# Kernel optimization log

Measured on AMD Instinct MI355X. Metric: run time of the kernel, lower is better.

## Reference

```python
import jax, jax.numpy as jnp
import numpy as np

DIM = 1024        # BIGNET_DIM
GS = 16           # group_size
N_LAYERS = 18     # 6 blocks * 3 QLoRALinear
N_BLOCKS = 6
R = 32            # lora_dim
B = 32768         # flattened batch/tokens
LN_EPS = 1e-5


def _qlora_linear(x, qw, sc, b, la, lb):
    # Dequantize int4 weights: per-group (group_size=16 along in_features) scale.
    O, I = qw.shape
    w = (qw.astype(jnp.float32).reshape(O, I // GS, GS) * sc[:, :, None]).reshape(O, I)
    base = x @ w.T + b                      # [B, O] dequant-matmul
    lora = (x @ la.T) @ lb.T                # fp32 low-rank branch [B,R]->[B,O]
    return base + lora


def _layernorm(x, g, b):
    mu = jnp.mean(x, axis=-1, keepdims=True)
    var = jnp.mean((x - mu) ** 2, axis=-1, keepdims=True)
    return (x - mu) * jax.lax.rsqrt(var + LN_EPS) * g + b


def setup_inputs() -> dict:
    key = jax.random.key(0)
    ks = jax.random.split(key, 6)
    x = jax.random.normal(ks[0], (B, DIM), dtype=jnp.float32)
    # int4 codes in [-8, 7]
    qw = jax.random.randint(ks[1], (N_LAYERS, DIM, DIM), -8, 8, dtype=jnp.int32)
    # positive per-group scales (absmax/7-like magnitude)
    scales = jax.random.uniform(ks[2], (N_LAYERS, DIM, DIM // GS), dtype=jnp.float32,
                                minval=0.005, maxval=0.02)
    bias = 0.02 * jax.random.normal(ks[3], (N_LAYERS, DIM), dtype=jnp.float32)
    lora_a = (1.0 / np.sqrt(DIM)) * jax.random.normal(ks[4], (N_LAYERS, R, DIM), dtype=jnp.float32)
    # lora_b is zero-init in the module; use small random values so the branch is exercised
    lora_b = 0.01 * jax.random.normal(ks[5], (N_LAYERS, DIM, R), dtype=jnp.float32)
    ln_g = jnp.ones((N_BLOCKS - 1, DIM), dtype=jnp.float32)
    ln_b = jnp.zeros((N_BLOCKS - 1, DIM), dtype=jnp.float32)
    return {"x": x, "qw": qw, "scales": scales, "bias": bias,
            "lora_a": lora_a, "lora_b": lora_b, "ln_g": ln_g, "ln_b": ln_b}


def reference(x, qw, scales, bias, lora_a, lora_b, ln_g, ln_b):
    h = x
    for blk in range(N_BLOCKS):
        y = h
        for j in range(3):
            li = blk * 3 + j
            y = _qlora_linear(y, qw[li], scales[li], bias[li], lora_a[li], lora_b[li])
            if j < 2:
                y = jax.nn.relu(y)
        h = y + h                     # residual
        if blk < N_BLOCKS - 1:
            h = _layernorm(h, ln_g[blk], ln_b[blk])
    return h
```

## Files before the change

### kernel.cpp

```cpp
#include <hip/hip_runtime.h>
#include <cstdint>

typedef _Float16 f16;
typedef _Float16 f16x8 __attribute__((ext_vector_type(8)));
typedef _Float16 f16x4 __attribute__((ext_vector_type(4)));
typedef float    f32x4 __attribute__((ext_vector_type(4)));

#define DIMN 1024
#define BATCH 32768
#define NLAYERS 18
#define NBLOCKS 6

__device__ __forceinline__ void gl2lds16(const f16* g, const f16* l) {
    auto gp = (const __attribute__((address_space(1))) unsigned int*)(uintptr_t)g;
    auto lp = (__attribute__((address_space(3))) unsigned int*)(uintptr_t)l;
    __builtin_amdgcn_global_load_lds(gp, lp, 16, 0, 0);
}

__global__ void cvt_kernel(const float* __restrict__ x, f16* __restrict__ o) {
    int i = (blockIdx.x * 256 + threadIdx.x) * 4;
    float4 v = *(const float4*)&x[i];
    f16x4 r;
    r[0] = (f16)v.x; r[1] = (f16)v.y; r[2] = (f16)v.z; r[3] = (f16)v.w;
    *(f16x4*)&o[i] = r;
}

__global__ __launch_bounds__(256) void prep_w_kernel(
        const int* __restrict__ qw, const float* __restrict__ sc,
        const float* __restrict__ la, const float* __restrict__ lb,
        f16* __restrict__ W) {
    int b = blockIdx.x;
    int li = b >> 7;
    int og = (b & 127) << 3;
    __shared__ float lbs[8][32];
    int tid = threadIdx.x;
    lbs[tid >> 5][tid & 31] = lb[((size_t)li * 1024 + og + (tid >> 5)) * 32 + (tid & 31)];
    __syncthreads();

    int i0 = tid * 4;
    const float* laL = la + (size_t)li * 32 * 1024;
    float acc[8][4] = {};
    for (int r = 0; r < 32; ++r) {
        float4 lav = *(const float4*)&laL[r * 1024 + i0];
#pragma unroll
        for (int q = 0; q < 8; ++q) {
            float wv = lbs[q][r];
            acc[q][0] += wv * lav.x; acc[q][1] += wv * lav.y;
            acc[q][2] += wv * lav.z; acc[q][3] += wv * lav.w;
        }
    }
#pragma unroll
    for (int q = 0; q < 8; ++q) {
        size_t row = (size_t)li * 1024 + og + q;
        size_t rowbase = row * 1024;
        int4 code = *(const int4*)&qw[rowbase + i0];
        float scale = sc[row * 64 + (i0 >> 4)];
        f16x4 o;
        o[0] = (f16)((float)code.x * scale + acc[q][0]);
        o[1] = (f16)((float)code.y * scale + acc[q][1]);
        o[2] = (f16)((float)code.z * scale + acc[q][2]);
        o[3] = (f16)((float)code.w * scale + acc[q][3]);
        *(f16x4*)&W[rowbase + i0] = o;
    }
}

__global__ __launch_bounds__(512, 2) void gemm_kernel(
        const f16* __restrict__ A, const f16* __restrict__ W,
        const float* __restrict__ bias, f16* __restrict__ C, int relu) {
    __shared__ __align__(16) char smem[131072];

    int tid = threadIdx.x;
    int l = tid & 63, w = tid >> 6;
    int wm = w >> 2, wn = w & 3;

    int hb = blockIdx.x;
    int xcd = hb & 7, idx = hb >> 3;
    int mt = xcd * 16 + (idx >> 2);
    int nt = idx & 3;
    int bm = mt * 256, bn = nt * 256;

    int ss = ((tid & 3) ^ ((tid >> 3) & 3)) * 8;
    const f16* Ag0 = A + (size_t)(bm + (tid >> 2)) * DIMN + ss;
    const f16* Ag1 = Ag0 + (size_t)128 * DIMN;
    const f16* Bg0 = W + (size_t)(bn + (tid >> 2)) * DIMN + ss;
    const f16* Bg1 = Bg0 + (size_t)128 * DIMN;
    int ldst = tid * 16;

    int lr = l & 15;
    int slot = ((l >> 4) ^ (lr >> 1)) & 3;
    int byteA = (wm * 128 + lr) * 64 + slot * 16;
    int byteB = (wn * 64 + lr) * 64 + slot * 16 + 16384;

    f32x4 acc[8][4] = {};

#pragma unroll
    for (int p = 0; p < 3; ++p) {
        char* bse = smem + p * 32768;
        gl2lds16(Ag0 + p * 32, (const f16*)(bse + ldst));
        gl2lds16(Ag1 + p * 32, (const f16*)(bse + 8192 + ldst));
        gl2lds16(Bg0 + p * 32, (const f16*)(bse + 16384 + ldst));
        gl2lds16(Bg1 + p * 32, (const f16*)(bse + 24576 + ldst));
    }
    asm volatile("s_waitcnt vmcnt(8)" ::: "memory");
    __builtin_amdgcn_s_barrier();
    asm volatile("" ::: "memory");

    for (int kt = 0; kt < 32; ++kt) {
        int kp = (kt + 3) & 31;
        char* bse = smem + ((kt + 3) & 3) * 32768;
        gl2lds16(Ag0 + kp * 32, (const f16*)(bse + ldst));
        gl2lds16(Ag1 + kp * 32, (const f16*)(bse + 8192 + ldst));
        gl2lds16(Bg0 + kp * 32, (const f16*)(bse + 16384 + ldst));
        gl2lds16(Bg1 + kp * 32, (const f16*)(bse + 24576 + ldst));

        const char* buf = smem + (kt & 3) * 32768;
        f16x8 af[8], bf[4];
#pragma unroll
        for (int m = 0; m < 8; ++m)
            af[m] = *(const f16x8*)(buf + byteA + m * 1024);
#pragma unroll
        for (int n = 0; n < 4; ++n)
            bf[n] = *(const f16x8*)(buf + byteB + n * 1024);

        __builtin_amdgcn_s_setprio(1);
#pragma unroll
        for (int m = 0; m < 8; ++m)
#pragma unroll
            for (int n = 0; n < 4; ++n)
                acc[m][n] = __builtin_amdgcn_mfma_f32_16x16x32_f16(
                    af[m], bf[n], acc[m][n], 0, 0, 0);
        __builtin_amdgcn_s_setprio(0);

        asm volatile("s_waitcnt vmcnt(8)" ::: "memory");
        __builtin_amdgcn_s_barrier();
        asm volatile("" ::: "memory");
    }

    __syncthreads();
    f16* Cs = (f16*)smem;
    const int LDC2 = 264;
    int gc = wn * 64 + lr;
    float bsv[4];
#pragma unroll
    for (int j = 0; j < 4; ++j) bsv[j] = bias[bn + gc + j * 16];
    int r0 = (l >> 4) * 4;
    int srow = tid >> 5, sc8 = (tid & 31) * 8;
#pragma unroll
    for (int half = 0; half < 2; ++half) {
        if (wm == half) {
#pragma unroll
            for (int m = 0; m < 8; ++m)
#pragma unroll
                for (int j = 0; j < 4; ++j)
#pragma unroll
                    for (int r = 0; r < 4; ++r) {
                        float v = acc[m][j][r] + bsv[j];
                        if (relu) v = fmaxf(v, 0.f);
                        Cs[(m * 16 + r0 + r) * LDC2 + gc + j * 16] = (f16)v;
                    }
        }
        __syncthreads();
#pragma unroll
        for (int it = 0; it < 8; ++it) {
            int row = srow + it * 16;
            f16x8 val = *(const f16x8*)&Cs[row * LDC2 + sc8];
            *(f16x8*)&C[(size_t)(bm + half * 128 + row) * DIMN + bn + sc8] = val;
        }
        if (half == 0) __syncthreads();
    }
}

__global__ void res_ln_kernel(const f16* __restrict__ y, f16* __restrict__ h,
                              const float* __restrict__ g, const float* __restrict__ b,
                              float* __restrict__ outF, int mode) {
    int row = blockIdx.x;
    int tid = threadIdx.x;
    int c0 = tid * 4;
    const f16* yr = y + (size_t)row * DIMN;
    f16* hr = h + (size_t)row * DIMN;

    f16x4 yv = *(const f16x4*)&yr[c0];
    f16x4 hv = *(const f16x4*)&hr[c0];
    float v[4];
    float s = 0.f, sq = 0.f;
#pragma unroll
    for (int i = 0; i < 4; ++i) {
        v[i] = (float)yv[i] + (float)hv[i];
        s += v[i]; sq += v[i] * v[i];
    }
#pragma unroll
    for (int o = 32; o > 0; o >>= 1) {
        s += __shfl_xor(s, o);
        sq += __shfl_xor(sq, o);
    }
    __shared__ float red[8];
    int wv = tid >> 6, ln = tid & 63;
    if (ln == 0) { red[wv] = s; red[4 + wv] = sq; }
    __syncthreads();
    float S1 = red[0] + red[1] + red[2] + red[3];
    float S2 = red[4] + red[5] + red[6] + red[7];
    float mu = S1 * (1.f / 1024.f);
    float var = S2 * (1.f / 1024.f) - mu * mu;
    float rs = rsqrtf(var + 1e-5f);

    if (mode == 0) {
        float4 gv = *(const float4*)&g[c0];
        float4 bv = *(const float4*)&b[c0];
        f16x4 outv;
        outv[0] = (f16)((v[0] - mu) * rs * gv.x + bv.x);
        outv[1] = (f16)((v[1] - mu) * rs * gv.y + bv.y);
        outv[2] = (f16)((v[2] - mu) * rs * gv.z + bv.z);
        outv[3] = (f16)((v[3] - mu) * rs * gv.w + bv.w);
        *(f16x4*)&hr[c0] = outv;
    } else {
        float4 ov;
        ov.x = v[0]; ov.y = v[1]; ov.z = v[2]; ov.w = v[3];
        *(float4*)&outF[(size_t)row * DIMN + c0] = ov;
    }
}

extern "C" void kernel_launch(void* const* d_in, const int* in_sizes, int n_in,
                              void* d_out, int out_size, void* d_ws, size_t ws_size,
                              hipStream_t stream) {
    const float* x    = (const float*)d_in[0];
    const int*   qw   = (const int*)d_in[1];
    const float* sc   = (const float*)d_in[2];
    const float* bias = (const float*)d_in[3];
    const float* la   = (const float*)d_in[4];
    const float* lb   = (const float*)d_in[5];
    const float* lng  = (const float*)d_in[6];
    const float* lnb  = (const float*)d_in[7];
    float* out = (float*)d_out;

    char* ws = (char*)d_ws;
    f16* Weff = (f16*)ws;
    f16* H    = (f16*)(ws + (size_t)37748736);
    f16* P    = (f16*)(ws + (size_t)37748736 + 67108864);
    f16* Q    = (f16*)d_out;

    cvt_kernel<<<BATCH * DIMN / (256 * 4), 256, 0, stream>>>(x, H);
    prep_w_kernel<<<NLAYERS * 128, 256, 0, stream>>>(qw, sc, la, lb, Weff);

    for (int blk = 0; blk < NBLOCKS; ++blk) {
        for (int j = 0; j < 3; ++j) {
            int li = blk * 3 + j;
            const f16* in = (j == 0) ? H : ((j == 1) ? P : Q);
            f16* o = (j == 1) ? Q : P;
            gemm_kernel<<<512, 512, 0, stream>>>(
                in, Weff + ((size_t)li << 20), bias + li * 1024, o, (j < 2) ? 1 : 0);
        }
        int lnidx = (blk < 5) ? blk : 4;
        res_ln_kernel<<<BATCH, 256, 0, stream>>>(
            P, H, lng + lnidx * 1024, lnb + lnidx * 1024, out, (blk == 5) ? 1 : 0);
    }
}
```

Baseline: 1.859 ms.

## Restructure GEMM mainloop into 8-phase ping-pong schedule with 64-wide K tiles

Rewrites the GEMM main loop so that each block stages K=64 slices into two 64KB LDS slots, split into half-tiles. Each iteration runs eight phases, and each phase interleaves LDS fragment loads, async global-to-LDS staging of the next half-tile, and one quadrant of MFMAs. Barriers, sched_barriers and setprio fence each phase. The warp tile is remapped into 2x2 quadrants with an 8-way XOR swizzle. The aim is to hide global-load and LDS latency behind MFMA work and to cut barrier count per K step. The cost is much more complex hand scheduling, with a risk of waitcnt/ordering mistakes and added register pressure.

Measured after the change: 1.773 ms. 4.6% less time.

```diff
diff --git a/kernel.cpp b/kernel.cpp
--- a/kernel.cpp
+++ b/kernel.cpp
@@ -72,6 +72,7 @@
     int tid = threadIdx.x;
     int l = tid & 63, w = tid >> 6;
     int wm = w >> 2, wn = w & 3;
+    int lr = l & 15;
 
     int hb = blockIdx.x;
     int xcd = hb & 7, idx = hb >> 3;
@@ -79,94 +80,123 @@
     int nt = idx & 3;
     int bm = mt * 256, bn = nt * 256;
 
-    int ss = ((tid & 3) ^ ((tid >> 3) & 3)) * 8;
-    const f16* Ag0 = A + (size_t)(bm + (tid >> 2)) * DIMN + ss;
-    const f16* Ag1 = Ag0 + (size_t)128 * DIMN;
-    const f16* Bg0 = W + (size_t)(bn + (tid >> 2)) * DIMN + ss;
-    const f16* Bg1 = Bg0 + (size_t)128 * DIMN;
-    int ldst = tid * 16;
-
-    int lr = l & 15;
-    int slot = ((l >> 4) ^ (lr >> 1)) & 3;
-    int byteA = (wm * 128 + lr) * 64 + slot * 16;
-    int byteB = (wn * 64 + lr) * 64 + slot * 16 + 16384;
-
-    f32x4 acc[8][4] = {};
-
-#pragma unroll
-    for (int p = 0; p < 3; ++p) {
-        char* bse = smem + p * 32768;
-        gl2lds16(Ag0 + p * 32, (const f16*)(bse + ldst));
-        gl2lds16(Ag1 + p * 32, (const f16*)(bse + 8192 + ldst));
-        gl2lds16(Bg0 + p * 32, (const f16*)(bse + 16384 + ldst));
-        gl2lds16(Bg1 + p * 32, (const f16*)(bse + 24576 + ldst));
-    }
-    asm volatile("s_waitcnt vmcnt(8)" ::: "memory");
+    int kswz = ((tid & 7) ^ ((tid >> 3) & 7)) * 8;
+    const f16* pA = A + (size_t)(bm + (tid >> 3)) * 1024 + kswz;
+    const f16* pB = W + (size_t)(bn + (tid >> 3)) * 1024 + kswz;
+    int ld0 = tid * 16;
+
+#define STG_A(SL, H, KOFF) do { \
+    gl2lds16(pA + ((size_t)((H)*128) << 10) + (KOFF), (const f16*)(smem + (SL)*65536 + (H)*16384 + ld0)); \
+    gl2lds16(pA + ((size_t)((H)*128+64) << 10) + (KOFF), (const f16*)(smem + (SL)*65536 + (H)*16384 + 8192 + ld0)); \
+  } while(0)
+#define STG_B(SL, H, KOFF) do { \
+    gl2lds16(pB + ((size_t)((H)*128) << 10) + (KOFF), (const f16*)(smem + (SL)*65536 + 32768 + (H)*16384 + ld0)); \
+    gl2lds16(pB + ((size_t)((H)*128+64) << 10) + (KOFF), (const f16*)(smem + (SL)*65536 + 32768 + (H)*16384 + 8192 + ld0)); \
+  } while(0)
+
+    int baseA = (wm * 64 + lr) * 128;
+    int baseB = 32768 + (wn * 32 + lr) * 128;
+    int slt0 = (((l >> 4) + 0) ^ (l & 7)) * 16;
+    int slt1 = (((l >> 4) + 4) ^ (l & 7)) * 16;
+
+    f16x8 af[4][2], bf[2][2];
+    f32x4 acc[2][2][4][2] = {};
+
+#define LDA(SL, MH) do { _Pragma("unroll") \
+    for (int mf = 0; mf < 4; ++mf) { \
+      af[mf][0] = *(const f16x8*)(smem + (SL)*65536 + (MH)*16384 + baseA + mf*2048 + slt0); \
+      af[mf][1] = *(const f16x8*)(smem + (SL)*65536 + (MH)*16384 + baseA + mf*2048 + slt1); \
+    } } while(0)
+#define LDB(SL, NH) do { _Pragma("unroll") \
+    for (int nf = 0; nf < 2; ++nf) { \
+      bf[nf][0] = *(const f16x8*)(smem + (SL)*65536 + (NH)*16384 + baseB + nf*2048 + slt0); \
+      bf[nf][1] = *(const f16x8*)(smem + (SL)*65536 + (NH)*16384 + baseB + nf*2048 + slt1); \
+    } } while(0)
+#define QMMA(MH, NH) do { _Pragma("unroll") \
+    for (int mf = 0; mf < 4; ++mf) { _Pragma("unroll") for (int nf = 0; nf < 2; ++nf) { \
+      acc[MH][NH][mf][nf] = __builtin_amdgcn_mfma_f32_16x16x32_f16(af[mf][0], bf[nf][0], acc[MH][NH][mf][nf], 0, 0, 0); \
+      acc[MH][NH][mf][nf] = __builtin_amdgcn_mfma_f32_16x16x32_f16(af[mf][1], bf[nf][1], acc[MH][NH][mf][nf], 0, 0, 0); \
+    } } } while(0)
+#define PH_TAIL do { \
+    __builtin_amdgcn_s_barrier(); \
+    asm volatile("s_waitcnt lgkmcnt(0)" ::: "memory"); \
+    __builtin_amdgcn_sched_barrier(0); \
+    __builtin_amdgcn_s_setprio(1); } while(0)
+#define PH_END do { \
+    __builtin_amdgcn_sched_barrier(0); \
+    __builtin_amdgcn_s_setprio(0); \
+    __builtin_amdgcn_s_barrier(); } while(0)
+
+    STG_B(0, 0, 0);
+    STG_A(0, 1, 0);
+    STG_A(0, 0, 0);
+    STG_B(0, 1, 0);
+    STG_B(1, 0, 64);
+    STG_A(1, 1, 64);
+    asm volatile("s_waitcnt vmcnt(4)" ::: "memory");
     __builtin_amdgcn_s_barrier();
-    asm volatile("" ::: "memory");
-
-    for (int kt = 0; kt < 32; ++kt) {
-        int kp = (kt + 3) & 31;
-        char* bse = smem + ((kt + 3) & 3) * 32768;
-        gl2lds16(Ag0 + kp * 32, (const f16*)(bse + ldst));
-        gl2lds16(Ag1 + kp * 32, (const f16*)(bse + 8192 + ldst));
-        gl2lds16(Bg0 + kp * 32, (const f16*)(bse + 16384 + ldst));
-        gl2lds16(Bg1 + kp * 32, (const f16*)(bse + 24576 + ldst));
-
-        const char* buf = smem + (kt & 3) * 32768;
-        f16x8 af[8], bf[4];
-#pragma unroll
-        for (int m = 0; m < 8; ++m)
-            af[m] = *(const f16x8*)(buf + byteA + m * 1024);
-#pragma unroll
-        for (int n = 0; n < 4; ++n)
-            bf[n] = *(const f16x8*)(buf + byteB + n * 1024);
-
-        __builtin_amdgcn_s_setprio(1);
-#pragma unroll
-        for (int m = 0; m < 8; ++m)
-#pragma unroll
-            for (int n = 0; n < 4; ++n)
-                acc[m][n] = __builtin_amdgcn_mfma_f32_16x16x32_f16(
-                    af[m], bf[n], acc[m][n], 0, 0, 0);
-        __builtin_amdgcn_s_setprio(0);
-
-        asm volatile("s_waitcnt vmcnt(8)" ::: "memory");
-        __builtin_amdgcn_s_barrier();
-        asm volatile("" ::: "memory");
-    }
-
+
+#pragma unroll 1
+    for (int i = 0; i < 8; ++i) {
+        int k1 = (2 * i + 1) * 64;
+        int k2 = ((2 * i + 2) & 15) * 64;
+        int k3 = ((2 * i + 3) & 15) * 64;
+        bool stg = (i < 7);
+        LDA(0, 0); LDB(0, 0); STG_A(1, 0, k1);
+        PH_TAIL; QMMA(0, 0); PH_END;
+        LDA(0, 1); STG_B(1, 1, k1);
+        PH_TAIL; QMMA(1, 0); PH_END;
+        LDB(0, 1); if (stg) STG_B(0, 0, k2);
+        PH_TAIL; QMMA(1, 1); PH_END;
+        LDA(0, 0); if (stg) STG_A(0, 1, k2);
+        if (i == 7) asm volatile("s_waitcnt vmcnt(0)" ::: "memory");
+        else        asm volatile("s_waitcnt vmcnt(4)" ::: "memory");
+        PH_TAIL; QMMA(0, 1); PH_END;
+        LDA(1, 0); LDB(1, 0); if (stg) STG_A(0, 0, k2);
+        PH_TAIL; QMMA(0, 0); PH_END;
+        LDA(1, 1); if (stg) STG_B(0, 1, k2);
+        PH_TAIL; QMMA(1, 0); PH_END;
+        LDB(1, 1); if (stg) STG_B(1, 0, k3);
+        PH_TAIL; QMMA(1, 1); PH_END;
+        LDA(1, 0); if (stg) STG_A(1, 1, k3);
+        asm volatile("s_waitcnt vmcnt(4)" ::: "memory");
+        PH_TAIL; QMMA(0, 1); PH_END;
+    }
+
+    asm volatile("s_waitcnt vmcnt(0)" ::: "memory");
     __syncthreads();
     f16* Cs = (f16*)smem;
     const int LDC2 = 264;
-    int gc = wn * 64 + lr;
-    float bsv[4];
-#pragma unroll
-    for (int j = 0; j < 4; ++j) bsv[j] = bias[bn + gc + j * 16];
+    float bsv[2][2];
+#pragma unroll
+    for (int nh = 0; nh < 2; ++nh)
+#pragma unroll
+        for (int nf = 0; nf < 2; ++nf)
+            bsv[nh][nf] = bias[bn + nh * 128 + wn * 32 + nf * 16 + lr];
     int r0 = (l >> 4) * 4;
-    int srow = tid >> 5, sc8 = (tid & 31) * 8;
-#pragma unroll
-    for (int half = 0; half < 2; ++half) {
-        if (wm == half) {
-#pragma unroll
-            for (int m = 0; m < 8; ++m)
-#pragma unroll
-                for (int j = 0; j < 4; ++j)
+    int c8 = (tid & 31) * 8, rr = tid >> 5;
+#pragma unroll
+    for (int mh = 0; mh < 2; ++mh) {
+#pragma unroll
+        for (int mf = 0; mf < 4; ++mf)
+#pragma unroll
+            for (int nh = 0; nh < 2; ++nh)
+#pragma unroll
+                for (int nf = 0; nf < 2; ++nf)
 #pragma unroll
                     for (int r = 0; r < 4; ++r) {
-                        float v = acc[m][j][r] + bsv[j];
+                        float v = acc[mh][nh][mf][nf][r] + bsv[nh][nf];
                         if (relu) v = fmaxf(v, 0.f);
-                        Cs[(m * 16 + r0 + r) * LDC2 + gc + j * 16] = (f16)v;
+                        Cs[(wm * 64 + mf * 16 + r0 + r) * LDC2 + nh * 128 + wn * 32 + nf * 16 + lr] = (f16)v;
                     }
+        __syncthreads();
+#pragma unroll
+        for (int it = 0; it < 8; ++it) {
+            int row = rr + it * 16;
+            f16x8 val = *(const f16x8*)&Cs[row * LDC2 + c8];
+            *(f16x8*)&C[(size_t)(bm + mh * 128 + row) * 1024 + bn + c8] = val;
         }
-        __syncthreads();
-#pragma unroll
-        for (int it = 0; it < 8; ++it) {
-            int row = srow + it * 16;
-            f16x8 val = *(const f16x8*)&Cs[row * LDC2 + sc8];
-            *(f16x8*)&C[(size_t)(bm + half * 128 + row) * DIMN + bn + sc8] = val;
-        }
-        if (half == 0) __syncthreads();
+        if (mh == 0) __syncthreads();
     }
 }
 
```

## Switch GEMM to 32x32x16 MFMA with split A/B staging and register double-buffering

Applied to the files above, without the earlier changes.

Replaces the 16x16x32 MFMA tiles with 32x32x16 instructions, using swapped operands so each lane's accumulator holds contiguous output columns. The main loop is restructured into half-step phases that double-buffer LDS fragment reads in registers, split the global-to-LDS staging of A and B across phases, and use fine-grained waitcnt plus sched_barriers so LDS reads overlap MFMA issue. The epilogue is rewritten to write packed f16x4 with vectorized bias loads. This adds scheduling complexity and register pressure in exchange for fewer LDS reads per MFMA and better overlap.

New measurement: 1.714 ms. 7.8% less time.

```diff
diff --git a/kernel.cpp b/kernel.cpp
--- a/kernel.cpp
+++ b/kernel.cpp
@@ -5,6 +5,7 @@
 typedef _Float16 f16x8 __attribute__((ext_vector_type(8)));
 typedef _Float16 f16x4 __attribute__((ext_vector_type(4)));
 typedef float    f32x4 __attribute__((ext_vector_type(4)));
+typedef float    f32x16 __attribute__((ext_vector_type(16)));
 
 #define DIMN 1024
 #define BATCH 32768
@@ -72,6 +73,9 @@
     int tid = threadIdx.x;
     int l = tid & 63, w = tid >> 6;
     int wm = w >> 2, wn = w & 3;
+    int m_l = l & 31;
+    int kg = l >> 5;
+    int flane = (m_l >> 1) & 3;
 
     int hb = blockIdx.x;
     int xcd = hb & 7, idx = hb >> 3;
@@ -79,94 +83,124 @@
     int nt = idx & 3;
     int bm = mt * 256, bn = nt * 256;
 
-    int ss = ((tid & 3) ^ ((tid >> 3) & 3)) * 8;
-    const f16* Ag0 = A + (size_t)(bm + (tid >> 2)) * DIMN + ss;
-    const f16* Ag1 = Ag0 + (size_t)128 * DIMN;
-    const f16* Bg0 = W + (size_t)(bn + (tid >> 2)) * DIMN + ss;
-    const f16* Bg1 = Bg0 + (size_t)128 * DIMN;
-    int ldst = tid * 16;
-
-    int lr = l & 15;
-    int slot = ((l >> 4) ^ (lr >> 1)) & 3;
-    int byteA = (wm * 128 + lr) * 64 + slot * 16;
-    int byteB = (wn * 64 + lr) * 64 + slot * 16 + 16384;
-
-    f32x4 acc[8][4] = {};
-
-#pragma unroll
-    for (int p = 0; p < 3; ++p) {
-        char* bse = smem + p * 32768;
-        gl2lds16(Ag0 + p * 32, (const f16*)(bse + ldst));
-        gl2lds16(Ag1 + p * 32, (const f16*)(bse + 8192 + ldst));
-        gl2lds16(Bg0 + p * 32, (const f16*)(bse + 16384 + ldst));
-        gl2lds16(Bg1 + p * 32, (const f16*)(bse + 24576 + ldst));
-    }
-    asm volatile("s_waitcnt vmcnt(8)" ::: "memory");
+    int trow = tid >> 2;
+    int ksrc = (tid & 3) ^ ((tid >> 3) & 3);
+    const f16* pA = A + (size_t)(bm + trow) * 1024 + ksrc * 8;
+    const f16* pB = W + (size_t)(bn + trow) * 1024 + ksrc * 8;
+    int ld0 = tid * 16;
+
+#define STGA(SL, KT) do { \
+    gl2lds16(pA + (KT) * 32, (const f16*)(smem + (SL) * 32768 + ld0)); \
+    gl2lds16(pA + 131072 + (KT) * 32, (const f16*)(smem + (SL) * 32768 + 8192 + ld0)); } while (0)
+#define STGB(SL, KT) do { \
+    gl2lds16(pB + (KT) * 32, (const f16*)(smem + (SL) * 32768 + 16384 + ld0)); \
+    gl2lds16(pB + 131072 + (KT) * 32, (const f16*)(smem + (SL) * 32768 + 24576 + ld0)); } while (0)
+
+    int aoff[4], boff[2];
+#pragma unroll
+    for (int mf = 0; mf < 4; ++mf) aoff[mf] = (wm * 128 + mf * 32 + m_l) * 64;
+#pragma unroll
+    for (int nf = 0; nf < 2; ++nf) boff[nf] = 16384 + (wn * 64 + nf * 32 + m_l) * 64;
+    int slt0 = ((0 + kg) ^ flane) * 16;
+    int slt1 = ((2 + kg) ^ flane) * 16;
+
+    f16x8 aE[4], bE[2], aO[4], bO[2];
+    f32x16 acc[4][2] = {};
+
+#define READS(DA, DB, SBASE, SLT) do { _Pragma("unroll") \
+    for (int mf = 0; mf < 4; ++mf) DA[mf] = *(const f16x8*)(smem + (SBASE) + aoff[mf] + (SLT)); \
+    _Pragma("unroll") \
+    for (int nf = 0; nf < 2; ++nf) DB[nf] = *(const f16x8*)(smem + (SBASE) + boff[nf] + (SLT)); } while (0)
+
+#define MMA8(AF, BF) do { _Pragma("unroll") \
+    for (int mf = 0; mf < 4; ++mf) { _Pragma("unroll") \
+      for (int nf = 0; nf < 2; ++nf) \
+        acc[mf][nf] = __builtin_amdgcn_mfma_f32_32x32x16_f16(BF[nf], AF[mf], acc[mf][nf], 0, 0, 0); } } while (0)
+
+#define WAITS do { \
+    asm volatile("s_waitcnt vmcnt(4) lgkmcnt(6)" ::: "memory"); \
+    __builtin_amdgcn_sched_barrier(0); \
+    __builtin_amdgcn_s_barrier(); \
+    __builtin_amdgcn_sched_barrier(0); } while (0)
+
+#define PHASES(T4, DT) do { \
+    int kp = ((T4) + (DT) + 3) & 31; \
+     \
+    READS(aO, bO, ((DT) & 3) * 32768, slt1); \
+    STGA(((DT) + 3) & 3, kp); \
+    WAITS; \
+    __builtin_amdgcn_s_setprio(1); \
+    MMA8(aE, bE); \
+    __builtin_amdgcn_s_setprio(0); \
+    __builtin_amdgcn_sched_barrier(0); \
+     \
+    READS(aE, bE, (((DT) + 1) & 3) * 32768, slt0); \
+    STGB(((DT) + 3) & 3, kp); \
+    WAITS; \
+    __builtin_amdgcn_s_setprio(1); \
+    MMA8(aO, bO); \
+    __builtin_amdgcn_s_setprio(0); \
+    __builtin_amdgcn_sched_barrier(0); \
+  } while (0)
+
+    STGA(0, 0); STGB(0, 0);
+    STGA(1, 1); STGB(1, 1);
+    STGA(2, 2); STGB(2, 2);
+    asm volatile("s_waitcnt vmcnt(4)" ::: "memory");
     __builtin_amdgcn_s_barrier();
-    asm volatile("" ::: "memory");
-
-    for (int kt = 0; kt < 32; ++kt) {
-        int kp = (kt + 3) & 31;
-        char* bse = smem + ((kt + 3) & 3) * 32768;
-        gl2lds16(Ag0 + kp * 32, (const f16*)(bse + ldst));
-        gl2lds16(Ag1 + kp * 32, (const f16*)(bse + 8192 + ldst));
-        gl2lds16(Bg0 + kp * 32, (const f16*)(bse + 16384 + ldst));
-        gl2lds16(Bg1 + kp * 32, (const f16*)(bse + 24576 + ldst));
-
-        const char* buf = smem + (kt & 3) * 32768;
-        f16x8 af[8], bf[4];
-#pragma unroll
-        for (int m = 0; m < 8; ++m)
-            af[m] = *(const f16x8*)(buf + byteA + m * 1024);
-#pragma unroll
-        for (int n = 0; n < 4; ++n)
-            bf[n] = *(const f16x8*)(buf + byteB + n * 1024);
-
-        __builtin_amdgcn_s_setprio(1);
-#pragma unroll
-        for (int m = 0; m < 8; ++m)
-#pragma unroll
-            for (int n = 0; n < 4; ++n)
-                acc[m][n] = __builtin_amdgcn_mfma_f32_16x16x32_f16(
-                    af[m], bf[n], acc[m][n], 0, 0, 0);
-        __builtin_amdgcn_s_setprio(0);
-
-        asm volatile("s_waitcnt vmcnt(8)" ::: "memory");
-        __builtin_amdgcn_s_barrier();
-        asm volatile("" ::: "memory");
+    READS(aE, bE, 0, slt0);
+
+#pragma unroll 1
+    for (int t4 = 0; t4 < 32; t4 += 4) {
+        PHASES(t4, 0);
+        PHASES(t4, 1);
+        PHASES(t4, 2);
+        PHASES(t4, 3);
     }
 
     __syncthreads();
     f16* Cs = (f16*)smem;
-    const int LDC2 = 264;
-    int gc = wn * 64 + lr;
-    float bsv[4];
-#pragma unroll
-    for (int j = 0; j < 4; ++j) bsv[j] = bias[bn + gc + j * 16];
-    int r0 = (l >> 4) * 4;
-    int srow = tid >> 5, sc8 = (tid & 31) * 8;
-#pragma unroll
-    for (int half = 0; half < 2; ++half) {
-        if (wm == half) {
-#pragma unroll
-            for (int m = 0; m < 8; ++m)
-#pragma unroll
-                for (int j = 0; j < 4; ++j)
-#pragma unroll
-                    for (int r = 0; r < 4; ++r) {
-                        float v = acc[m][j][r] + bsv[j];
-                        if (relu) v = fmaxf(v, 0.f);
-                        Cs[(m * 16 + r0 + r) * LDC2 + gc + j * 16] = (f16)v;
+    float4 bsv[2][4];
+#pragma unroll
+    for (int nf = 0; nf < 2; ++nf)
+#pragma unroll
+        for (int g = 0; g < 4; ++g)
+            bsv[nf][g] = *(const float4*)&bias[bn + wn * 64 + nf * 32 + g * 8 + kg * 4];
+
+    int c8 = (tid & 31) * 8, rr = tid >> 5;
+#pragma unroll
+    for (int pass = 0; pass < 2; ++pass) {
+        if (wm == pass) {
+#pragma unroll
+            for (int mf = 0; mf < 4; ++mf) {
+                int row = mf * 32 + m_l;
+#pragma unroll
+                for (int nf = 0; nf < 2; ++nf)
+#pragma unroll
+                    for (int g = 0; g < 4; ++g) {
+                        float4 vb = bsv[nf][g];
+                        float v0 = acc[mf][nf][g * 4 + 0] + vb.x;
+                        float v1 = acc[mf][nf][g * 4 + 1] + vb.y;
+                        float v2 = acc[mf][nf][g * 4 + 2] + vb.z;
+                        float v3 = acc[mf][nf][g * 4 + 3] + vb.w;
+                        if (relu) {
+                            v0 = fmaxf(v0, 0.f); v1 = fmaxf(v1, 0.f);
+                            v2 = fmaxf(v2, 0.f); v3 = fmaxf(v3, 0.f);
+                        }
+                        f16x4 pk;
+                        pk[0] = (f16)v0; pk[1] = (f16)v1; pk[2] = (f16)v2; pk[3] = (f16)v3;
+                        *(f16x4*)&Cs[row * 264 + wn * 64 + nf * 32 + g * 8 + kg * 4] = pk;
                     }
+            }
         }
         __syncthreads();
 #pragma unroll
         for (int it = 0; it < 8; ++it) {
-            int row = srow + it * 16;
-            f16x8 val = *(const f16x8*)&Cs[row * LDC2 + sc8];
-            *(f16x8*)&C[(size_t)(bm + half * 128 + row) * DIMN + bn + sc8] = val;
-        }
-        if (half == 0) __syncthreads();
+            int rowr = rr + it * 16;
+            f16x8 val = *(const f16x8*)&Cs[rowr * 264 + c8];
+            *(f16x8*)&C[(size_t)(bm + pass * 128 + rowr) * 1024 + bn + c8] = val;
+        }
+        if (pass == 0) __syncthreads();
     }
 }
 
```
